# Optimization experiments

Hardware: AMD Instinct MI355X
Metric: run time of the kernel (lower is better)

The kernel has to match this reference:

```python
import jax, jax.numpy as jnp
import numpy as np

B, J, N = 64, 32, 4096
Q_DIM, K_DIM, V_DIM, H = 130, 128, 130, 4


def _init_linear(key, fan_in, fan_out):
    kw, kb = jax.random.split(key)
    bound = 1.0 / np.sqrt(fan_in)
    W = jax.random.uniform(kw, (fan_in, fan_out), jnp.float32, -bound, bound)
    b = jax.random.uniform(kb, (fan_out,), jnp.float32, -bound, bound)
    return W, b


def setup_inputs() -> dict:
    key = jax.random.key(0)
    ks = jax.random.split(key, 10)
    joint_q = jax.random.normal(ks[0], (B, J, Q_DIM), jnp.float32)
    vertex_k = jax.random.normal(ks[1], (B, N, K_DIM), jnp.float32)
    vertex_v = jax.random.normal(ks[2], (B, N, V_DIM), jnp.float32)
    vertex_mask = jax.random.bernoulli(ks[3], 0.1, (B, N))  # True = masked
    # joint_q_encoder: Linear(130,64) ReLU Linear(64, 128*4)
    W1, b1 = _init_linear(ks[4], Q_DIM, 64)
    W2, b2 = _init_linear(ks[5], 64, K_DIM * H)
    # joint_output_layer: Linear(520,64) ReLU Linear(64,32) ReLU Linear(32,1)
    W3, b3 = _init_linear(ks[6], V_DIM * H, 64)
    W4, b4 = _init_linear(ks[7], 64, 32)
    W5, b5 = _init_linear(ks[8], 32, 1)
    return {
        "joint_q": joint_q, "vertex_k": vertex_k, "vertex_v": vertex_v,
        "vertex_mask": vertex_mask,
        "W1": W1, "b1": b1, "W2": W2, "b2": b2,
        "W3": W3, "b3": b3, "W4": W4, "b4": b4, "W5": W5, "b5": b5,
    }


def reference(joint_q, vertex_k, vertex_v, vertex_mask,
              W1, b1, W2, b2, W3, b3, W4, b4, W5, b5):
    b, j, _ = joint_q.shape
    # Encode queries: [B,J,130] -> [B,J,H,K]
    h = jax.nn.relu(joint_q @ W1 + b1)
    q = (h @ W2 + b2).reshape(b, j, H, K_DIM)
    # Attention scores via broadcasted contraction (avoids materializing
    # the expanded K/V copies the torch code builds): [B,J,H,N]
    scores = jnp.einsum('bjhk,bnk->bjhn', q, vertex_k) / np.sqrt(K_DIM).astype(np.float32)
    scores = jnp.where(vertex_mask[:, None, None, :], jnp.float32(-1e9), scores)
    attn = jax.nn.softmax(scores, axis=-1)
    # Weighted values: [B,J,H,V] -> [B,J,H*V]
    out = jnp.einsum('bjhn,bnv->bjhv', attn, vertex_v).reshape(b, j, H * V_DIM)
    # Output MLP -> [B,J]
    out = jax.nn.relu(out @ W3 + b3)
    out = jax.nn.relu(out @ W4 + b4)
    out = (out @ W5 + b5).squeeze(-1)
    return out
```

## Files before the change

kernel.cpp:

```cpp
#include <hip/hip_runtime.h>
#include <hip/hip_bf16.h>

#define BB 64
#define JJ 32
#define NN 4096
#define QD 130
#define KD 128
#define VD 130
#define HH 4
#define CT 8
#define NCH (NN / CT)
#define TIL (NCH / 32)
#define PSTRIDE (JJ + JJ + JJ * VD)

typedef __attribute__((ext_vector_type(8)))  __bf16 bf16x8;
typedef __attribute__((ext_vector_type(16))) float  f32x16;

union FW4 { unsigned int u[4]; bf16x8 v; };

#define SEL_HI 0x07060302u

__device__ __forceinline__ unsigned int packhi(float f0, float f1) {
    return __builtin_amdgcn_perm(__float_as_uint(f1), __float_as_uint(f0), SEL_HI);
}
__device__ __forceinline__ float truncbf(float f) {
    return __uint_as_float(__float_as_uint(f) & 0xFFFF0000u);
}
__device__ __forceinline__ void split8(float4 a, float4 b, bf16x8* h, bf16x8* l) {
    FW4 H, L;
    H.u[0] = packhi(a.x, a.y);
    H.u[1] = packhi(a.z, a.w);
    H.u[2] = packhi(b.x, b.y);
    H.u[3] = packhi(b.z, b.w);
    L.u[0] = packhi(a.x - truncbf(a.x), a.y - truncbf(a.y));
    L.u[1] = packhi(a.z - truncbf(a.z), a.w - truncbf(a.w));
    L.u[2] = packhi(b.x - truncbf(b.x), b.y - truncbf(b.y));
    L.u[3] = packhi(b.z - truncbf(b.z), b.w - truncbf(b.w));
    *h = H.v; *l = L.v;
}

__global__ __launch_bounds__(64) void enc_kernel(
        const float* __restrict__ jq,
        const float* __restrict__ W1, const float* __restrict__ b1,
        const float* __restrict__ W2, const float* __restrict__ b2,
        float* __restrict__ qenc) {
    int row = blockIdx.x;
    int t = threadIdx.x;
    __shared__ float x[QD];
    __shared__ float h[64];
    for (int i = t; i < QD; i += 64) x[i] = jq[row * QD + i];
    __syncthreads();
    float a0 = 0.f, a1 = 0.f;
    for (int i = 0; i < QD - 1; i += 2) {
        a0 += x[i] * W1[i * 64 + t];
        a1 += x[i + 1] * W1[(i + 1) * 64 + t];
    }
    h[t] = fmaxf(b1[t] + a0 + a1, 0.f);
    __syncthreads();
    float a[8];
    #pragma unroll
    for (int s = 0; s < 8; ++s) a[s] = b2[t + 64 * s];
    for (int i = 0; i < 64; ++i) {
        float hv = h[i];
        #pragma unroll
        for (int s = 0; s < 8; ++s) a[s] += hv * W2[i * 512 + t + 64 * s];
    }
    #pragma unroll
    for (int s = 0; s < 8; ++s) qenc[row * 512 + t + 64 * s] = a[s];
}

__global__ __launch_bounds__(512, 2) void attn_kernel(
        const float* __restrict__ Kg, const float* __restrict__ Vg,
        const int* __restrict__ maskg, const float* __restrict__ qenc,
        float* __restrict__ part) {
    int blk = blockIdx.x;
    int c = blk & (CT - 1);
    int b = blk / CT;
    int tid = threadIdx.x;
    int wid = tid >> 6;
    int lane = tid & 63;
    int l31 = lane & 31;
    int lh = lane >> 5;

    __shared__ __align__(16) __bf16 Kbf[2][2][8][64][8];
    __shared__ __align__(16) __bf16 Vbf[2][2][8][64][8];
    __shared__ float Vtc[2][2][32];
    __shared__ int   msks[2][32];
    __shared__ float r_lds[4][32];

    const float* Kb = Kg + (size_t)b * NN * KD;
    const float* Vb = Vg + (size_t)b * NN * VD;
    const int*   Mb = maskg + b * NN;

    if (wid >= 4) {
        int sid = tid - 256;
        int sl = sid & 63;
        int grp = sid >> 6;
        const int kstA = grp, kstB = grp + 4;
        const int gB = grp + 4;
        const int vAcol = (grp >> 1) * 32 + (sl & 31);
        const int vArow = (grp & 1) * 16 + (sl >> 5) * 8;
        const int vBcol = (gB >> 1) * 32 + (sl & 31);
        const int vBrow = (gB & 1) * 16 + (sl >> 5) * 8;

        float k0a[8], k0b[8], v0a[8], v0b[8]; float2 vt0 = {0, 0}; int mk0 = 0;
        float k1a[8], k1b[8], v1a[8], v1b[8]; float2 vt1 = {0, 0}; int mk1 = 0;

        auto sload = [&](float* kA, float* kB2, float* vA, float* vB2,
                         float2& vt, int& mk, int T) {
            int n0 = c * NCH + T * 32;
            const float* ka = Kb + (size_t)(n0 + (sl & 31)) * KD + kstA * 16 + (sl >> 5) * 8;
            *(float4*)&kA[0] = *(const float4*)ka;
            *(float4*)&kA[4] = *(const float4*)(ka + 4);
            const float* kb2 = Kb + (size_t)(n0 + (sl & 31)) * KD + kstB * 16 + (sl >> 5) * 8;
            *(float4*)&kB2[0] = *(const float4*)kb2;
            *(float4*)&kB2[4] = *(const float4*)(kb2 + 4);
            const float* va = Vb + (size_t)(n0 + vArow) * VD + vAcol;
            #pragma unroll
            for (int j = 0; j < 8; ++j) vA[j] = va[(size_t)j * VD];
            const float* vb = Vb + (size_t)(n0 + vBrow) * VD + vBcol;
            #pragma unroll
            for (int j = 0; j < 8; ++j) vB2[j] = vb[(size_t)j * VD];
            if (sid < 32) {
                vt = *(const float2*)(Vb + (size_t)(n0 + sid) * VD + 128);
                mk = Mb[n0 + sid];
            }
        };
        auto ssplit = [&](float* kA, float* kB2, float* vA, float* vB2,
                          float2 vt, int mk, int BUF) {
            bf16x8 h, l;
            split8(*(float4*)&kA[0], *(float4*)&kA[4], &h, &l);
            *(bf16x8*)&Kbf[BUF][0][kstA][sl][0] = h;
            *(bf16x8*)&Kbf[BUF][1][kstA][sl][0] = l;
            split8(*(float4*)&kB2[0], *(float4*)&kB2[4], &h, &l);
            *(bf16x8*)&Kbf[BUF][0][kstB][sl][0] = h;
            *(bf16x8*)&Kbf[BUF][1][kstB][sl][0] = l;
            split8(*(float4*)&vA[0], *(float4*)&vA[4], &h, &l);
            *(bf16x8*)&Vbf[BUF][0][grp][sl][0] = h;
            *(bf16x8*)&Vbf[BUF][1][grp][sl][0] = l;
            split8(*(float4*)&vB2[0], *(float4*)&vB2[4], &h, &l);
            *(bf16x8*)&Vbf[BUF][0][gB][sl][0] = h;
            *(bf16x8*)&Vbf[BUF][1][gB][sl][0] = l;
            if (sid < 32) {
                Vtc[BUF][0][sid] = vt.x;
                Vtc[BUF][1][sid] = vt.y;
                msks[BUF][sid] = mk;
            }
        };

        sload(k0a, k0b, v0a, v0b, vt0, mk0, 0);
        sload(k1a, k1b, v1a, v1b, vt1, mk1, 1);
        ssplit(k0a, k0b, v0a, v0b, vt0, mk0, 0);
        __syncthreads();

        for (int t = 0; t < TIL; ++t) {
            if ((t & 1) == 0) {
                if (t + 2 < TIL) sload(k0a, k0b, v0a, v0b, vt0, mk0, t + 2);
                ssplit(k1a, k1b, v1a, v1b, vt1, mk1, 1);
            } else {
                if (t + 2 < TIL) sload(k1a, k1b, v1a, v1b, vt1, mk1, t + 2);
                if (t + 1 < TIL) ssplit(k0a, k0b, v0a, v0b, vt0, mk0, 0);
            }
            __syncthreads();
        }
    } else {
        bf16x8 qh[8], ql[8];
        {
            const float* qrow = qenc + (size_t)(b * JJ + l31) * 512 + wid * KD + lh * 8;
            #pragma unroll
            for (int kst = 0; kst < 8; ++kst) {
                float4 qa = *(const float4*)(qrow + kst * 16);
                float4 qb = *(const float4*)(qrow + kst * 16 + 4);
                split8(qa, qb, &qh[kst], &ql[kst]);
            }
        }

        f32x16 O[4];
        #pragma unroll
        for (int vt = 0; vt < 4; ++vt)
            #pragma unroll
            for (int r = 0; r < 16; ++r) O[vt][r] = 0.f;
        float acct0 = 0.f, acct1 = 0.f;
        float m_run = -1e30f, l_run = 0.f;

        __syncthreads();

        for (int t = 0; t < TIL; ++t) {
            int cur = t & 1;

            int mv = msks[cur][l31];
            unsigned int mword = (unsigned int)__ballot(mv != 0);

            f32x16 S0, S1;
            #pragma unroll
            for (int r = 0; r < 16; ++r) { S0[r] = 0.f; S1[r] = 0.f; }
            #pragma unroll
            for (int kst = 0; kst < 4; ++kst) {
                bf16x8 kh = *(const bf16x8*)&Kbf[cur][0][kst][lane][0];
                bf16x8 kl = *(const bf16x8*)&Kbf[cur][1][kst][lane][0];
                S0 = __builtin_amdgcn_mfma_f32_32x32x16_bf16(kh, qh[kst], S0, 0, 0, 0);
                S0 = __builtin_amdgcn_mfma_f32_32x32x16_bf16(kh, ql[kst], S0, 0, 0, 0);
                S0 = __builtin_amdgcn_mfma_f32_32x32x16_bf16(kl, qh[kst], S0, 0, 0, 0);
            }
            #pragma unroll
            for (int kst = 4; kst < 8; ++kst) {
                bf16x8 kh = *(const bf16x8*)&Kbf[cur][0][kst][lane][0];
                bf16x8 kl = *(const bf16x8*)&Kbf[cur][1][kst][lane][0];
                S1 = __builtin_amdgcn_mfma_f32_32x32x16_bf16(kh, qh[kst], S1, 0, 0, 0);
                S1 = __builtin_amdgcn_mfma_f32_32x32x16_bf16(kh, ql[kst], S1, 0, 0, 0);
                S1 = __builtin_amdgcn_mfma_f32_32x32x16_bf16(kl, qh[kst], S1, 0, 0, 0);
            }

            const float sc = 0.08838834764831845f;
            float sp[16];
            float rm = -1e30f;
            #pragma unroll
            for (int r = 0; r < 16; ++r) {
                int key = (r & 3) + 8 * (r >> 2) + (lh << 2);
                float s = ((mword >> key) & 1u) ? -1e30f : (S0[r] + S1[r]) * sc;
                sp[r] = s;
                rm = fmaxf(rm, s);
            }
            rm = fmaxf(rm, __shfl_xor(rm, 32));
            if (!__all(rm <= m_run + 8.f)) {
                float mn = fmaxf(m_run, rm);
                float rs = __expf(m_run - mn);
                m_run = mn;
                l_run *= rs; acct0 *= rs; acct1 *= rs;
                if (lane < 32) r_lds[wid][lane] = rs;
                float rr[16];
                #pragma unroll
                for (int r = 0; r < 16; ++r)
                    rr[r] = r_lds[wid][(r & 3) + 8 * (r >> 2) + (lh << 2)];
                #pragma unroll
                for (int vt = 0; vt < 4; ++vt)
                    #pragma unroll
                    for (int r = 0; r < 16; ++r) O[vt][r] *= rr[r];
            }
            float ps = 0.f;
            #pragma unroll
            for (int r = 0; r < 16; ++r) {
                float p = __expf(sp[r] - m_run);
                sp[r] = p;
                ps += p;
            }
            ps += __shfl_xor(ps, 32);
            l_run += ps;

            #pragma unroll
            for (int r = 0; r < 16; ++r) {
                int key = (r & 3) + 8 * (r >> 2) + (lh << 2);
                acct0 += sp[r] * Vtc[cur][0][key];
                acct1 += sp[r] * Vtc[cur][1][key];
            }

            bf16x8 pah[2], pal[2];
            #pragma unroll
            for (int ks = 0; ks < 2; ++ks) {
                int b0 = 8 * ks;
                unsigned int wh[4], wl[4];
                #pragma unroll
                for (int i = 0; i < 4; ++i) {
                    float p0 = sp[b0 + 2 * i], p1 = sp[b0 + 2 * i + 1];
                    wh[i] = packhi(p0, p1);
                    wl[i] = packhi(p0 - truncbf(p0), p1 - truncbf(p1));
                }
                unsigned int s0h = __shfl_xor(wh[0], 32), s1h = __shfl_xor(wh[1], 32);
                unsigned int s2h = __shfl_xor(wh[2], 32), s3h = __shfl_xor(wh[3], 32);
                unsigned int s0l = __shfl_xor(wl[0], 32), s1l = __shfl_xor(wl[1], 32);
                unsigned int s2l = __shfl_xor(wl[2], 32), s3l = __shfl_xor(wl[3], 32);
                FW4 PH, PL;
                PH.u[0] = lh ? s2h : wh[0];
                PH.u[1] = lh ? s3h : wh[1];
                PH.u[2] = lh ? wh[2] : s0h;
                PH.u[3] = lh ? wh[3] : s1h;
                PL.u[0] = lh ? s2l : wl[0];
                PL.u[1] = lh ? s3l : wl[1];
                PL.u[2] = lh ? wl[2] : s0l;
                PL.u[3] = lh ? wl[3] : s1l;
                pah[ks] = PH.v; pal[ks] = PL.v;
            }

            #pragma unroll
            for (int ks = 0; ks < 2; ++ks) {
                #pragma unroll
                for (int vt = 0; vt < 4; ++vt) {
                    int g = vt * 2 + ks;
                    bf16x8 vh = *(const bf16x8*)&Vbf[cur][0][g][lane][0];
                    bf16x8 vl = *(const bf16x8*)&Vbf[cur][1][g][lane][0];
                    O[vt] = __builtin_amdgcn_mfma_f32_32x32x16_bf16(pah[ks], vh, O[vt], 0, 0, 0);
                    O[vt] = __builtin_amdgcn_mfma_f32_32x32x16_bf16(pal[ks], vh, O[vt], 0, 0, 0);
                    O[vt] = __builtin_amdgcn_mfma_f32_32x32x16_bf16(pah[ks], vl, O[vt], 0, 0, 0);
                }
            }

            __syncthreads();
        }

        float* P = part + (size_t)((b * HH + wid) * CT + c) * PSTRIDE;
        if (lane < 32) { P[lane] = m_run; P[JJ + lane] = l_run; }
        float* A = P + 2 * JJ;
        #pragma unroll
        for (int vt = 0; vt < 4; ++vt) {
            #pragma unroll
            for (int r = 0; r < 16; ++r) {
                int q = (r & 3) + 8 * (r >> 2) + (lh << 2);
                A[q * VD + vt * 32 + l31] = O[vt][r];
            }
        }
        float t0 = acct0 + __shfl_xor(acct0, 32);
        float t1 = acct1 + __shfl_xor(acct1, 32);
        if (lh == 0) {
            A[l31 * VD + 128] = t0;
            A[l31 * VD + 129] = t1;
        }
    }
}

__global__ __launch_bounds__(64) void comb_mlp_kernel(
        const float* __restrict__ part,
        const float* __restrict__ W3, const float* __restrict__ b3,
        const float* __restrict__ W4, const float* __restrict__ b4,
        const float* __restrict__ W5, const float* __restrict__ b5,
        float* __restrict__ out) {
    int row = blockIdx.x;
    int b = row >> 5;
    int j = row & 31;
    int t = threadIdx.x;
    __shared__ float w_s[HH][CT];
    __shared__ float x[HH * VD];
    __shared__ float h1[64];
    __shared__ float h2[32];

    if (t < HH * CT) {
        int h = t / CT, cc = t % CT;
        const float* P = part + (size_t)((b * HH + h) * CT + cc) * PSTRIDE;
        float m = P[j];
        float l = P[JJ + j];
        float mm = m;
        #pragma unroll
        for (int s = 1; s < CT; s <<= 1) mm = fmaxf(mm, __shfl_xor(mm, s));
        float e = __expf(m - mm);
        float L = l * e;
        #pragma unroll
        for (int s = 1; s < CT; s <<= 1) L += __shfl_xor(L, s);
        w_s[h][cc] = (L > 0.f) ? e / L : 0.f;
    }
    __syncthreads();

    for (int idx = t; idx < HH * VD; idx += 64) {
        int h = idx / VD, v = idx - h * VD;
        const float* A = part + (size_t)(b * HH + h) * CT * PSTRIDE + 2 * JJ + j * VD + v;
        float o = 0.f;
        #pragma unroll 4
        for (int cc = 0; cc < CT; ++cc) o += w_s[h][cc] * A[(size_t)cc * PSTRIDE];
        x[idx] = o;
    }
    __syncthreads();

    float a0 = 0.f, a1 = 0.f, a2 = 0.f, a3 = 0.f;
    for (int i = 0; i < HH * VD; i += 4) {
        a0 += x[i] * W3[i * 64 + t];
        a1 += x[i + 1] * W3[(i + 1) * 64 + t];
        a2 += x[i + 2] * W3[(i + 2) * 64 + t];
        a3 += x[i + 3] * W3[(i + 3) * 64 + t];
    }
    h1[t] = fmaxf(b3[t] + (a0 + a1) + (a2 + a3), 0.f);
    __syncthreads();
    if (t < 32) {
        float c0 = 0.f, c1 = 0.f;
        for (int i = 0; i < 64; i += 2) {
            c0 += h1[i] * W4[i * 32 + t];
            c1 += h1[i + 1] * W4[(i + 1) * 32 + t];
        }
        h2[t] = fmaxf(b4[t] + c0 + c1, 0.f);
    }
    __syncthreads();
    if (t == 0) {
        float a3f = b5[0];
        for (int i = 0; i < 32; ++i) a3f += h2[i] * W5[i];
        out[row] = a3f;
    }
}

extern "C" void kernel_launch(void* const* d_in, const int* in_sizes, int n_in,
                              void* d_out, int out_size, void* d_ws, size_t ws_size,
                              hipStream_t stream) {
    const float* jq = (const float*)d_in[0];
    const float* Kg = (const float*)d_in[1];
    const float* Vg = (const float*)d_in[2];
    const int* mask = (const int*)d_in[3];
    const float* W1 = (const float*)d_in[4];
    const float* b1 = (const float*)d_in[5];
    const float* W2 = (const float*)d_in[6];
    const float* b2 = (const float*)d_in[7];
    const float* W3 = (const float*)d_in[8];
    const float* b3 = (const float*)d_in[9];
    const float* W4 = (const float*)d_in[10];
    const float* b4 = (const float*)d_in[11];
    const float* W5 = (const float*)d_in[12];
    const float* b5 = (const float*)d_in[13];
    float* out = (float*)d_out;

    float* ws = (float*)d_ws;
    float* qenc = ws;
    float* part = qenc + (size_t)BB * JJ * HH * KD;

    enc_kernel<<<BB * JJ, 64, 0, stream>>>(jq, W1, b1, W2, b2, qenc);
    attn_kernel<<<BB * CT, 512, 0, stream>>>(Kg, Vg, mask, qenc, part);
    comb_mlp_kernel<<<BB * JJ, 64, 0, stream>>>(part, W3, b3, W4, b4, W5, b5, out);
}
```

Baseline: 118.8 us.

## Replace producer/consumer warp split with all-wave 16x16 MFMA attention and in-loop staging

```diff
diff --git a/kernel.cpp b/kernel.cpp
--- a/kernel.cpp
+++ b/kernel.cpp
@@ -13,8 +13,8 @@
 #define TIL (NCH / 32)
 #define PSTRIDE (JJ + JJ + JJ * VD)
 
-typedef __attribute__((ext_vector_type(8)))  __bf16 bf16x8;
-typedef __attribute__((ext_vector_type(16))) float  f32x16;
+typedef __attribute__((ext_vector_type(8))) __bf16 bf16x8;
+typedef __attribute__((ext_vector_type(4))) float  f32x4;
 
 union FW4 { unsigned int u[4]; bf16x8 v; };
 
@@ -69,7 +69,7 @@
     for (int s = 0; s < 8; ++s) qenc[row * 512 + t + 64 * s] = a[s];
 }
 
-__global__ __launch_bounds__(512, 2) void attn_kernel(
+__global__ __launch_bounds__(512, 4) void attn_kernel(
         const float* __restrict__ Kg, const float* __restrict__ Vg,
         const int* __restrict__ maskg, const float* __restrict__ qenc,
         float* __restrict__ part) {
@@ -79,241 +79,230 @@
     int tid = threadIdx.x;
     int wid = tid >> 6;
     int lane = tid & 63;
-    int l31 = lane & 31;
-    int lh = lane >> 5;
-
-    __shared__ __align__(16) __bf16 Kbf[2][2][8][64][8];
-    __shared__ __align__(16) __bf16 Vbf[2][2][8][64][8];
-    __shared__ float Vtc[2][2][32];
+    int h = wid & 3;
+    int qhalf = wid >> 2;
+    int g = lane >> 4;
+    int q15 = lane & 15;
+
+    __shared__ __align__(16) __bf16 Kf[2][2][2][4][65][8];
+    __shared__ __align__(16) __bf16 Vf[2][2][8][64][8];
+    __shared__ float Vt_s[2][2][32];
     __shared__ int   msks[2][32];
-    __shared__ float r_lds[4][32];
+
+    int skey = tid >> 4;
+    int sdhi = tid & 15;
+    int skh = skey >> 4, skst = sdhi >> 2;
+    int slK = (skey & 15) + 16 * (sdhi & 3);
+    int sv = tid & 127, skb = tid >> 7;
+    int svc = sv >> 4;
+    int slV = (sv & 15) + 16 * skb;
 
     const float* Kb = Kg + (size_t)b * NN * KD;
     const float* Vb = Vg + (size_t)b * NN * VD;
     const int*   Mb = maskg + b * NN;
 
-    if (wid >= 4) {
-        int sid = tid - 256;
-        int sl = sid & 63;
-        int grp = sid >> 6;
-        const int kstA = grp, kstB = grp + 4;
-        const int gB = grp + 4;
-        const int vAcol = (grp >> 1) * 32 + (sl & 31);
-        const int vArow = (grp & 1) * 16 + (sl >> 5) * 8;
-        const int vBcol = (gB >> 1) * 32 + (sl & 31);
-        const int vBrow = (gB & 1) * 16 + (sl >> 5) * 8;
-
-        float k0a[8], k0b[8], v0a[8], v0b[8]; float2 vt0 = {0, 0}; int mk0 = 0;
-        float k1a[8], k1b[8], v1a[8], v1b[8]; float2 vt1 = {0, 0}; int mk1 = 0;
-
-        auto sload = [&](float* kA, float* kB2, float* vA, float* vB2,
-                         float2& vt, int& mk, int T) {
-            int n0 = c * NCH + T * 32;
-            const float* ka = Kb + (size_t)(n0 + (sl & 31)) * KD + kstA * 16 + (sl >> 5) * 8;
-            *(float4*)&kA[0] = *(const float4*)ka;
-            *(float4*)&kA[4] = *(const float4*)(ka + 4);
-            const float* kb2 = Kb + (size_t)(n0 + (sl & 31)) * KD + kstB * 16 + (sl >> 5) * 8;
-            *(float4*)&kB2[0] = *(const float4*)kb2;
-            *(float4*)&kB2[4] = *(const float4*)(kb2 + 4);
-            const float* va = Vb + (size_t)(n0 + vArow) * VD + vAcol;
+    float4 kfa, kfb;
+    float  vf[8];
+    float2 vt = {0.f, 0.f};
+    int    mk = 0;
+
+    auto sload = [&](int T) {
+        int n0 = c * NCH + T * 32;
+        const float* ks = Kb + (size_t)(n0 + skey) * KD + sdhi * 8;
+        kfa = *(const float4*)ks;
+        kfb = *(const float4*)(ks + 4);
+        const float* vs = Vb + (size_t)(n0 + skb * 8) * VD + sv;
+        #pragma unroll
+        for (int j = 0; j < 8; ++j) vf[j] = vs[(size_t)j * VD];
+        if (tid < 32) {
+            vt = *(const float2*)(Vb + (size_t)(n0 + tid) * VD + 128);
+            mk = Mb[n0 + tid];
+        }
+    };
+    auto swrite = [&](int buf) {
+        bf16x8 hh, ll;
+        split8(kfa, kfb, &hh, &ll);
+        *(bf16x8*)&Kf[buf][0][skh][skst][slK][0] = hh;
+        *(bf16x8*)&Kf[buf][1][skh][skst][slK][0] = ll;
+        float4 va = {vf[0], vf[1], vf[2], vf[3]};
+        float4 vb2 = {vf[4], vf[5], vf[6], vf[7]};
+        split8(va, vb2, &hh, &ll);
+        *(bf16x8*)&Vf[buf][0][svc][slV][0] = hh;
+        *(bf16x8*)&Vf[buf][1][svc][slV][0] = ll;
+        if (tid < 32) {
+            Vt_s[buf][0][tid] = vt.x;
+            Vt_s[buf][1][tid] = vt.y;
+            msks[buf][tid] = mk;
+        }
+    };
+
+    sload(0);
+
+    bf16x8 qh[4], ql[4];
+    {
+        const float* qrow = qenc + (size_t)(b * JJ + qhalf * 16 + q15) * 512
+                            + h * KD + g * 8;
+        #pragma unroll
+        for (int kst = 0; kst < 4; ++kst) {
+            float4 qa = *(const float4*)(qrow + kst * 32);
+            float4 qb = *(const float4*)(qrow + kst * 32 + 4);
+            split8(qa, qb, &qh[kst], &ql[kst]);
+        }
+    }
+
+    swrite(0);
+    sload(1);
+    __builtin_amdgcn_sched_barrier(0);
+
+    f32x4 O[8];
+    #pragma unroll
+    for (int vc = 0; vc < 8; ++vc)
+        #pragma unroll
+        for (int r = 0; r < 4; ++r) O[vc][r] = 0.f;
+    float acct0 = 0.f, acct1 = 0.f;
+    float m_run = -1e30f, l_run = 0.f;
+
+    __syncthreads();
+
+    for (int t = 0; t < TIL; ++t) {
+        int cur = t & 1;
+
+        if (t + 1 < TIL) {
+            swrite(cur ^ 1);
+            int T2 = (t + 2 < TIL) ? (t + 2) : t;
+            sload(T2);
+        }
+        __builtin_amdgcn_sched_barrier(0);
+
+        unsigned int mword = (unsigned int)__ballot(msks[cur][lane & 31] != 0);
+
+        f32x4 S[2];
+        #pragma unroll
+        for (int kh = 0; kh < 2; ++kh)
             #pragma unroll
-            for (int j = 0; j < 8; ++j) vA[j] = va[(size_t)j * VD];
-            const float* vb = Vb + (size_t)(n0 + vBrow) * VD + vBcol;
+            for (int r = 0; r < 4; ++r) S[kh][r] = 0.f;
+        #pragma unroll
+        for (int kst = 0; kst < 4; ++kst) {
             #pragma unroll
-            for (int j = 0; j < 8; ++j) vB2[j] = vb[(size_t)j * VD];
-            if (sid < 32) {
-                vt = *(const float2*)(Vb + (size_t)(n0 + sid) * VD + 128);
-                mk = Mb[n0 + sid];
+            for (int kh = 0; kh < 2; ++kh) {
+                bf16x8 khf = *(const bf16x8*)&Kf[cur][0][kh][kst][lane][0];
+                bf16x8 klf = *(const bf16x8*)&Kf[cur][1][kh][kst][lane][0];
+                S[kh] = __builtin_amdgcn_mfma_f32_16x16x32_bf16(khf, qh[kst], S[kh], 0, 0, 0);
+                S[kh] = __builtin_amdgcn_mfma_f32_16x16x32_bf16(khf, ql[kst], S[kh], 0, 0, 0);
+                S[kh] = __builtin_amdgcn_mfma_f32_16x16x32_bf16(klf, qh[kst], S[kh], 0, 0, 0);
             }
-        };
-        auto ssplit = [&](float* kA, float* kB2, float* vA, float* vB2,
-                          float2 vt, int mk, int BUF) {
-            bf16x8 h, l;
-            split8(*(float4*)&kA[0], *(float4*)&kA[4], &h, &l);
-            *(bf16x8*)&Kbf[BUF][0][kstA][sl][0] = h;
-            *(bf16x8*)&Kbf[BUF][1][kstA][sl][0] = l;
-            split8(*(float4*)&kB2[0], *(float4*)&kB2[4], &h, &l);
-            *(bf16x8*)&Kbf[BUF][0][kstB][sl][0] = h;
-            *(bf16x8*)&Kbf[BUF][1][kstB][sl][0] = l;
-            split8(*(float4*)&vA[0], *(float4*)&vA[4], &h, &l);
-            *(bf16x8*)&Vbf[BUF][0][grp][sl][0] = h;
-            *(bf16x8*)&Vbf[BUF][1][grp][sl][0] = l;
-            split8(*(float4*)&vB2[0], *(float4*)&vB2[4], &h, &l);
-            *(bf16x8*)&Vbf[BUF][0][gB][sl][0] = h;
-            *(bf16x8*)&Vbf[BUF][1][gB][sl][0] = l;
-            if (sid < 32) {
-                Vtc[BUF][0][sid] = vt.x;
-                Vtc[BUF][1][sid] = vt.y;
-                msks[BUF][sid] = mk;
-            }
-        };
-
-        sload(k0a, k0b, v0a, v0b, vt0, mk0, 0);
-        sload(k1a, k1b, v1a, v1b, vt1, mk1, 1);
-        ssplit(k0a, k0b, v0a, v0b, vt0, mk0, 0);
-        __syncthreads();
-
-        for (int t = 0; t < TIL; ++t) {
-            if ((t & 1) == 0) {
-                if (t + 2 < TIL) sload(k0a, k0b, v0a, v0b, vt0, mk0, t + 2);
-                ssplit(k1a, k1b, v1a, v1b, vt1, mk1, 1);
-            } else {
-                if (t + 2 < TIL) sload(k1a, k1b, v1a, v1b, vt1, mk1, t + 2);
-                if (t + 1 < TIL) ssplit(k0a, k0b, v0a, v0b, vt0, mk0, 0);
-            }
-            __syncthreads();
-        }
-    } else {
-        bf16x8 qh[8], ql[8];
-        {
-            const float* qrow = qenc + (size_t)(b * JJ + l31) * 512 + wid * KD + lh * 8;
+        }
+
+        const float sc = 0.08838834764831845f;
+        float sp[8];
+        float rm = -1e30f;
+        #pragma unroll
+        for (int kh = 0; kh < 2; ++kh) {
             #pragma unroll
-            for (int kst = 0; kst < 8; ++kst) {
-                float4 qa = *(const float4*)(qrow + kst * 16);
-                float4 qb = *(const float4*)(qrow + kst * 16 + 4);
-                split8(qa, qb, &qh[kst], &ql[kst]);
-            }
-        }
-
-        f32x16 O[4];
-        #pragma unroll
-        for (int vt = 0; vt < 4; ++vt)
-            #pragma unroll
-            for (int r = 0; r < 16; ++r) O[vt][r] = 0.f;
-        float acct0 = 0.f, acct1 = 0.f;
-        float m_run = -1e30f, l_run = 0.f;
-
-        __syncthreads();
-
-        for (int t = 0; t < TIL; ++t) {
-            int cur = t & 1;
-
-            int mv = msks[cur][l31];
-            unsigned int mword = (unsigned int)__ballot(mv != 0);
-
-            f32x16 S0, S1;
-            #pragma unroll
-            for (int r = 0; r < 16; ++r) { S0[r] = 0.f; S1[r] = 0.f; }
-            #pragma unroll
-            for (int kst = 0; kst < 4; ++kst) {
-                bf16x8 kh = *(const bf16x8*)&Kbf[cur][0][kst][lane][0];
-                bf16x8 kl = *(const bf16x8*)&Kbf[cur][1][kst][lane][0];
-                S0 = __builtin_amdgcn_mfma_f32_32x32x16_bf16(kh, qh[kst], S0, 0, 0, 0);
-                S0 = __builtin_amdgcn_mfma_f32_32x32x16_bf16(kh, ql[kst], S0, 0, 0, 0);
-                S0 = __builtin_amdgcn_mfma_f32_32x32x16_bf16(kl, qh[kst], S0, 0, 0, 0);
-            }
-            #pragma unroll
-            for (int kst = 4; kst < 8; ++kst) {
-                bf16x8 kh = *(const bf16x8*)&Kbf[cur][0][kst][lane][0];
-                bf16x8 kl = *(const bf16x8*)&Kbf[cur][1][kst][lane][0];
-                S1 = __builtin_amdgcn_mfma_f32_32x32x16_bf16(kh, qh[kst], S1, 0, 0, 0);
-                S1 = __builtin_amdgcn_mfma_f32_32x32x16_bf16(kh, ql[kst], S1, 0, 0, 0);
-                S1 = __builtin_amdgcn_mfma_f32_32x32x16_bf16(kl, qh[kst], S1, 0, 0, 0);
-            }
-
-            const float sc = 0.08838834764831845f;
-            float sp[16];
-            float rm = -1e30f;
-            #pragma unroll
-            for (int r = 0; r < 16; ++r) {
-                int key = (r & 3) + 8 * (r >> 2) + (lh << 2);
-                float s = ((mword >> key) & 1u) ? -1e30f : (S0[r] + S1[r]) * sc;
-                sp[r] = s;
+            for (int r = 0; r < 4; ++r) {
+                int key = kh * 16 + g * 4 + r;
+                float s = ((mword >> key) & 1u) ? -1e30f : S[kh][r] * sc;
+                sp[kh * 4 + r] = s;
                 rm = fmaxf(rm, s);
             }
-            rm = fmaxf(rm, __shfl_xor(rm, 32));
-            if (!__all(rm <= m_run + 8.f)) {
-                float mn = fmaxf(m_run, rm);
-                float rs = __expf(m_run - mn);
-                m_run = mn;
-                l_run *= rs; acct0 *= rs; acct1 *= rs;
-                if (lane < 32) r_lds[wid][lane] = rs;
-                float rr[16];
+        }
+        rm = fmaxf(rm, __shfl_xor(rm, 16));
+        rm = fmaxf(rm, __shfl_xor(rm, 32));
+        if (!__all(rm <= m_run + 8.f)) {
+            float mn = fmaxf(m_run, rm);
+            float rs = __expf(m_run - mn);
+            m_run = mn;
+            l_run *= rs; acct0 *= rs; acct1 *= rs;
+            #pragma unroll
+            for (int r = 0; r < 4; ++r) {
+                float rr = __shfl(rs, g * 4 + r);
                 #pragma unroll
-                for (int r = 0; r < 16; ++r)
-                    rr[r] = r_lds[wid][(r & 3) + 8 * (r >> 2) + (lh << 2)];
-                #pragma unroll
-                for (int vt = 0; vt < 4; ++vt)
-                    #pragma unroll
-                    for (int r = 0; r < 16; ++r) O[vt][r] *= rr[r];
+                for (int vc = 0; vc < 8; ++vc) O[vc][r] *= rr;
             }
-            float ps = 0.f;
+        }
+        float ps = 0.f;
+        #pragma unroll
+        for (int i = 0; i < 8; ++i) {
+            float p = __expf(sp[i] - m_run);
+            sp[i] = p;
+            ps += p;
+        }
+        ps += __shfl_xor(ps, 16);
+        ps += __shfl_xor(ps, 32);
+        l_run += ps;
+
+        #pragma unroll
+        for (int kh = 0; kh < 2; ++kh) {
             #pragma unroll
-            for (int r = 0; r < 16; ++r) {
-                float p = __expf(sp[r] - m_run);
-                sp[r] = p;
-                ps += p;
+            for (int r = 0; r < 4; ++r) {
+                int key = kh * 16 + g * 4 + r;
+                acct0 += sp[kh * 4 + r] * Vt_s[cur][0][key];
+                acct1 += sp[kh * 4 + r] * Vt_s[cur][1][key];
             }
-            ps += __shfl_xor(ps, 32);
-            l_run += ps;
-
-            #pragma unroll
-            for (int r = 0; r < 16; ++r) {
-                int key = (r & 3) + 8 * (r >> 2) + (lh << 2);
-                acct0 += sp[r] * Vtc[cur][0][key];
-                acct1 += sp[r] * Vtc[cur][1][key];
-            }
-
-            bf16x8 pah[2], pal[2];
-            #pragma unroll
-            for (int ks = 0; ks < 2; ++ks) {
-                int b0 = 8 * ks;
-                unsigned int wh[4], wl[4];
-                #pragma unroll
-                for (int i = 0; i < 4; ++i) {
-                    float p0 = sp[b0 + 2 * i], p1 = sp[b0 + 2 * i + 1];
-                    wh[i] = packhi(p0, p1);
-                    wl[i] = packhi(p0 - truncbf(p0), p1 - truncbf(p1));
-                }
-                unsigned int s0h = __shfl_xor(wh[0], 32), s1h = __shfl_xor(wh[1], 32);
-                unsigned int s2h = __shfl_xor(wh[2], 32), s3h = __shfl_xor(wh[3], 32);
-                unsigned int s0l = __shfl_xor(wl[0], 32), s1l = __shfl_xor(wl[1], 32);
-                unsigned int s2l = __shfl_xor(wl[2], 32), s3l = __shfl_xor(wl[3], 32);
-                FW4 PH, PL;
-                PH.u[0] = lh ? s2h : wh[0];
-                PH.u[1] = lh ? s3h : wh[1];
-                PH.u[2] = lh ? wh[2] : s0h;
-                PH.u[3] = lh ? wh[3] : s1h;
-                PL.u[0] = lh ? s2l : wl[0];
-                PL.u[1] = lh ? s3l : wl[1];
-                PL.u[2] = lh ? wl[2] : s0l;
-                PL.u[3] = lh ? wl[3] : s1l;
-                pah[ks] = PH.v; pal[ks] = PL.v;
-            }
-
-            #pragma unroll
-            for (int ks = 0; ks < 2; ++ks) {
-                #pragma unroll
-                for (int vt = 0; vt < 4; ++vt) {
-                    int g = vt * 2 + ks;
-                    bf16x8 vh = *(const bf16x8*)&Vbf[cur][0][g][lane][0];
-                    bf16x8 vl = *(const bf16x8*)&Vbf[cur][1][g][lane][0];
-                    O[vt] = __builtin_amdgcn_mfma_f32_32x32x16_bf16(pah[ks], vh, O[vt], 0, 0, 0);
-                    O[vt] = __builtin_amdgcn_mfma_f32_32x32x16_bf16(pal[ks], vh, O[vt], 0, 0, 0);
-                    O[vt] = __builtin_amdgcn_mfma_f32_32x32x16_bf16(pah[ks], vl, O[vt], 0, 0, 0);
-                }
-            }
-
-            __syncthreads();
-        }
-
-        float* P = part + (size_t)((b * HH + wid) * CT + c) * PSTRIDE;
-        if (lane < 32) { P[lane] = m_run; P[JJ + lane] = l_run; }
-        float* A = P + 2 * JJ;
-        #pragma unroll
-        for (int vt = 0; vt < 4; ++vt) {
-            #pragma unroll
-            for (int r = 0; r < 16; ++r) {
-                int q = (r & 3) + 8 * (r >> 2) + (lh << 2);
-                A[q * VD + vt * 32 + l31] = O[vt][r];
-            }
-        }
-        float t0 = acct0 + __shfl_xor(acct0, 32);
-        float t1 = acct1 + __shfl_xor(acct1, 32);
-        if (lh == 0) {
-            A[l31 * VD + 128] = t0;
-            A[l31 * VD + 129] = t1;
-        }
+        }
+
+        unsigned u0h = packhi(sp[0], sp[1]), u1h = packhi(sp[2], sp[3]);
+        unsigned u2h = packhi(sp[4], sp[5]), u3h = packhi(sp[6], sp[7]);
+        unsigned u0l = packhi(sp[0] - truncbf(sp[0]), sp[1] - truncbf(sp[1]));
+        unsigned u1l = packhi(sp[2] - truncbf(sp[2]), sp[3] - truncbf(sp[3]));
+        unsigned u2l = packhi(sp[4] - truncbf(sp[4]), sp[5] - truncbf(sp[5]));
+        unsigned u3l = packhi(sp[6] - truncbf(sp[6]), sp[7] - truncbf(sp[7]));
+        int srcA = q15 + 32 * (g & 1);
+        int srcB = srcA + 16;
+        bool hiSel = (g >> 1) != 0;
+        unsigned a0 = __shfl(u0h, srcA), a1 = __shfl(u1h, srcA);
+        unsigned c0 = __shfl(u2h, srcA), c1 = __shfl(u3h, srcA);
+        unsigned a2 = __shfl(u0h, srcB), a3 = __shfl(u1h, srcB);
+        unsigned c2 = __shfl(u2h, srcB), c3 = __shfl(u3h, srcB);
+        FW4 PH;
+        PH.u[0] = hiSel ? c0 : a0;
+        PH.u[1] = hiSel ? c1 : a1;
+        PH.u[2] = hiSel ? c2 : a2;
+        PH.u[3] = hiSel ? c3 : a3;
+        unsigned e0 = __shfl(u0l, srcA), e1 = __shfl(u1l, srcA);
+        unsigned f0 = __shfl(u2l, srcA), f1 = __shfl(u3l, srcA);
+        unsigned e2 = __shfl(u0l, srcB), e3 = __shfl(u1l, srcB);
+        unsigned f2 = __shfl(u2l, srcB), f3 = __shfl(u3l, srcB);
+        FW4 PL;
+        PL.u[0] = hiSel ? f0 : e0;
+        PL.u[1] = hiSel ? f1 : e1;
+        PL.u[2] = hiSel ? f2 : e2;
+        PL.u[3] = hiSel ? f3 : e3;
+        bf16x8 PAH = PH.v, PAL = PL.v;
+
+        #pragma unroll
+        for (int vc = 0; vc < 8; ++vc) {
+            bf16x8 vh = *(const bf16x8*)&Vf[cur][0][vc][lane][0];
+            bf16x8 vl = *(const bf16x8*)&Vf[cur][1][vc][lane][0];
+            O[vc] = __builtin_amdgcn_mfma_f32_16x16x32_bf16(PAH, vh, O[vc], 0, 0, 0);
+            O[vc] = __builtin_amdgcn_mfma_f32_16x16x32_bf16(PAL, vh, O[vc], 0, 0, 0);
+            O[vc] = __builtin_amdgcn_mfma_f32_16x16x32_bf16(PAH, vl, O[vc], 0, 0, 0);
+        }
+
+        __syncthreads();
+    }
+
+    float* P = part + (size_t)((b * HH + h) * CT + c) * PSTRIDE;
+    if (lane < 16) {
+        P[qhalf * 16 + lane] = m_run;
+        P[JJ + qhalf * 16 + lane] = l_run;
+    }
+    float* A = P + 2 * JJ;
+    #pragma unroll
+    for (int vc = 0; vc < 8; ++vc) {
+        #pragma unroll
+        for (int r = 0; r < 4; ++r) {
+            int q = qhalf * 16 + g * 4 + r;
+            A[q * VD + vc * 16 + q15] = O[vc][r];
+        }
+    }
+    acct0 += __shfl_xor(acct0, 16);
+    acct0 += __shfl_xor(acct0, 32);
+    acct1 += __shfl_xor(acct1, 16);
+    acct1 += __shfl_xor(acct1, 32);
+    if (lane < 16) {
+        A[(qhalf * 16 + lane) * VD + 128] = acct0;
+        A[(qhalf * 16 + lane) * VD + 129] = acct1;
     }
 }
 
```

Result: slower. 170.7 us (+43.7%).
